# Kernel optimization log

Measured on AMD Instinct MI355X. Metric: run time of the kernel, lower is better.

## Reference

```python
import jax, jax.numpy as jnp
import numpy as np

H = 256  # hidden_size


def _lstm_cell(x, h, c, Wih, Whh, b):
    # PyTorch gate order: input, forget, cell(g), output
    gates = x @ Wih.T + h @ Whh.T + b  # (B, 4H)
    i, f, g, o = jnp.split(gates, 4, axis=-1)
    c_new = jax.nn.sigmoid(f) * c + jax.nn.sigmoid(i) * jnp.tanh(g)
    h_new = jax.nn.sigmoid(o) * jnp.tanh(c_new)
    return h_new, c_new


def setup_inputs() -> dict:
    key = jax.random.key(0)
    ks = jax.random.split(key, 9)
    B, D_in, T, H4 = 64, 64, 1024, 4 * H
    s = 0.05  # keep gates out of saturation
    return {
        "x": jax.random.normal(ks[0], (B, D_in, T), jnp.float32),
        # layer 0: input size 64; layers 1-2: input size 2*H (bidirectional concat)
        "Wih0": jax.random.normal(ks[1], (2, H4, D_in), jnp.float32) * s,
        "Whh0": jax.random.normal(ks[2], (2, H4, H), jnp.float32) * s,
        "b0": jax.random.normal(ks[3], (2, H4), jnp.float32) * s,  # b_ih + b_hh fused
        "Wih12": jax.random.normal(ks[4], (2, 2, H4, 2 * H), jnp.float32) * s,
        "Whh12": jax.random.normal(ks[5], (2, 2, H4, H), jnp.float32) * s,
        "b12": jax.random.normal(ks[6], (2, 2, H4), jnp.float32) * s,
        # Conv1d(1, 81, (256,1)) == per-timestep linear over the hidden dim
        "conv_w": jax.random.normal(ks[7], (81, H), jnp.float32) * s,
        "conv_b": jax.random.normal(ks[8], (81,), jnp.float32) * s,
    }


def reference(x, Wih0, Whh0, b0, Wih12, Whh12, b12, conv_w, conv_b):
    B = x.shape[0]
    seq = jnp.transpose(x, (2, 0, 1))  # (T, B, D_in) like x.permute(2,0,1)
    h0 = jnp.zeros((6, B, H), x.dtype)  # num_layers * num_directions = 6
    c0 = jnp.zeros((6, B, H), x.dtype)

    def step(carry, x_t):
        h, c = carry
        hs, cs = [], []
        inp = x_t  # single timestep fed to the (bi)LSTM: both dirs see the same input
        for l in range(3):
            outs = []
            for d in range(2):
                idx = 2 * l + d
                if l == 0:
                    Wih, Whh, b = Wih0[d], Whh0[d], b0[d]
                else:
                    Wih, Whh, b = Wih12[l - 1, d], Whh12[l - 1, d], b12[l - 1, d]
                hn, cn = _lstm_cell(inp, h[idx], c[idx], Wih, Whh, b)
                outs.append(hn)
                hs.append(hn)
                cs.append(cn)
            inp = jnp.concatenate(outs, axis=-1)  # (B, 2H) into next layer
        new_h = jnp.stack(hs)
        new_c = jnp.stack(cs)
        # h.view(L, 2, B, H)[-1, -1]: last layer, backward direction
        return (new_h, new_c), hs[-1]

    _, ys = jax.lax.scan(step, (h0, c0), seq)  # ys: (T, B, H)

    # y.permute(1,2,0).unsqueeze(1) -> conv (256,1) kernel -> squeeze(2):
    # logits[b, o, t] = sum_h conv_w[o, h] * ys[t, b, h] + conv_b[o]
    logits = jnp.einsum('tbh,oh->bot', ys, conv_w) + conv_b[None, :, None]
    probs = jax.nn.softmax(logits, axis=1)
    return jnp.argmax(probs, axis=1)  # (B, T) int
```

## Files before the change

### kernel.cpp

```cpp
#include <hip/hip_runtime.h>


#define H_ 256
#define B_ 64
#define T_ 1024
#define NBLK 256
#define NTHR 1024
#define HBUF 98304
#define NTICK 1026

#define OFF_GEN  0
#define OFF_ROOT 64
#define OFF_CNT  128
#define OFF_H    4096
#define OFF_XT   1048576
#define OFF_YS   17825792

__device__ __forceinline__ float sigf(float x) {
  return 1.0f / (1.0f + __expf(-x));
}
__device__ __forceinline__ float tanhf_(float x) {
  float e = __expf(-2.0f * fabsf(x));
  float r = (1.0f - e) / (1.0f + e);
  return x >= 0.0f ? r : -r;
}

__device__ __forceinline__ void llc_ld1(const float4* p, float4& r) {
  asm volatile(
      "global_load_dwordx4 %0, %1, off sc0 sc1\n\t"
      "s_waitcnt vmcnt(0)"
      : "=v"(r)
      : "v"(p)
      : "memory");
}
__device__ __forceinline__ void llc_ld4(const float4* p, float4& r0, float4& r1,
                                        float4& r2, float4& r3) {
  asm volatile(
      "global_load_dwordx4 %0, %4, off sc0 sc1\n\t"
      "global_load_dwordx4 %1, %4, off offset:1024 sc0 sc1\n\t"
      "global_load_dwordx4 %2, %4, off offset:2048 sc0 sc1\n\t"
      "global_load_dwordx4 %3, %4, off offset:3072 sc0 sc1\n\t"
      "s_waitcnt vmcnt(0)"
      : "=&v"(r0), "=&v"(r1), "=&v"(r2), "=&v"(r3)
      : "v"(p)
      : "memory");
}
__device__ __forceinline__ void llc_st1(float* p, float v) {
  asm volatile(
      "global_store_dword %0, %1, off sc0 sc1\n\t"
      "s_waitcnt vmcnt(0)" ::"v"(p),
      "v"(v)
      : "memory");
}
__device__ __forceinline__ void llc_st2(float* p1, float v1, float* p2, float v2) {
  asm volatile(
      "global_store_dword %0, %1, off sc0 sc1\n\t"
      "global_store_dword %2, %3, off sc0 sc1\n\t"
      "s_waitcnt vmcnt(0)" ::"v"(p1),
      "v"(v1), "v"(p2), "v"(v2)
      : "memory");
}

__global__ __launch_bounds__(64) void transpose_x(const float* __restrict__ x,
                                                  float* __restrict__ xT) {
  __shared__ float tile[64][65];
  const int k = blockIdx.y;
  const int t0 = blockIdx.x * 64;
  const int lane = threadIdx.x;
  for (int bi = 0; bi < 64; ++bi)
    tile[bi][lane] = x[bi * 65536 + k * 1024 + t0 + lane];
  __syncthreads();
  for (int ti = 0; ti < 64; ++ti)
    xT[(size_t)(t0 + ti) * 4096 + (k >> 2) * 256 + lane * 4 + (k & 3)] =
        tile[lane][ti];
}

__device__ __forceinline__ void body8(float* __restrict__ acc, const float4 av,
                                      const float* __restrict__ wb,
                                      const int ws, const int u0, const int k4) {
#pragma unroll
  for (int a = 0; a < 8; ++a) {
    const float* wp =
        wb + (size_t)((a & 3) * 256 + u0 + (a >> 2)) * ws + k4 * 4;
    float4 wq = *(const float4*)wp;
    acc[a] += wq.x * av.x + wq.y * av.y + wq.z * av.z + wq.w * av.w;
  }
}

__device__ __forceinline__ void seg8(float* __restrict__ acc, const int a,
                                     const int b, const float4* __restrict__ act,
                                     const int actOff,
                                     const float* __restrict__ wb, const int ws,
                                     const int u0, const int lane,
                                     const bool byp) {
  int k4 = a;
  for (; k4 + 4 <= b; k4 += 4) {
    const float4* p = act + (size_t)(k4 - actOff) * 64 + lane;
    float4 v0, v1, v2, v3;
    if (byp) {
      llc_ld4(p, v0, v1, v2, v3);
    } else {
      v0 = p[0];
      v1 = p[64];
      v2 = p[128];
      v3 = p[192];
    }
    body8(acc, v0, wb, ws, u0, k4 - actOff + 0);
    body8(acc, v1, wb, ws, u0, k4 - actOff + 1);
    body8(acc, v2, wb, ws, u0, k4 - actOff + 2);
    body8(acc, v3, wb, ws, u0, k4 - actOff + 3);
  }
  for (; k4 < b; ++k4) {
    const float4* p = act + (size_t)(k4 - actOff) * 64 + lane;
    float4 v;
    if (byp)
      llc_ld1(p, v);
    else
      v = *p;
    body8(acc, v, wb, ws, u0, k4 - actOff);
  }
}

__device__ __forceinline__ void task8(
    const int w, const int lane, const int tid, const int u0,
    const int K4, const int nA4,
    const float4* __restrict__ actA, const bool bypA,
    const float4* __restrict__ actB, const bool bypB,
    const float* __restrict__ wAb, const int wAs,
    const float* __restrict__ wBb, const int wBs,
    const float* __restrict__ bias,
    float* __restrict__ cst2,
    float* __restrict__ hcell,
    float* __restrict__ ysrow,
    float (*red)[64][12], const bool lastTask) {
  const int slice = K4 >> 4;
  const int lo = w * slice, hi = lo + slice;
  float acc[8] = {0.f, 0.f, 0.f, 0.f, 0.f, 0.f, 0.f, 0.f};

  {
    const int b4 = hi < nA4 ? hi : nA4;
    if (lo < b4) seg8(acc, lo, b4, actA, 0, wAb, wAs, u0, lane, bypA);
  }
  {
    const int a4 = lo > nA4 ? lo : nA4;
    if (a4 < hi) seg8(acc, a4, hi, actB, nA4, wBb, wBs, u0, lane, bypB);
  }

  *(float4*)&red[w][lane][0] = make_float4(acc[0], acc[1], acc[2], acc[3]);
  *(float4*)&red[w][lane][4] = make_float4(acc[4], acc[5], acc[6], acc[7]);
  __syncthreads();

  if (tid < 128) {
    const int uu = tid >> 6, b = tid & 63;
    float gi = bias[0 * 256 + u0 + uu];
    float gf = bias[1 * 256 + u0 + uu];
    float gg = bias[2 * 256 + u0 + uu];
    float go = bias[3 * 256 + u0 + uu];
#pragma unroll
    for (int ww = 0; ww < 16; ++ww) {
      float4 s = *(const float4*)&red[ww][b][uu * 4];
      gi += s.x; gf += s.y; gg += s.z; go += s.w;
    }
    float iv = sigf(gi), fv = sigf(gf), gv = tanhf_(gg), ov = sigf(go);
    float c = fv * cst2[uu * 64 + b] + iv * gv;
    cst2[uu * 64 + b] = c;
    float h = ov * tanhf_(c);
    const int u = u0 + uu;
    float* hp = hcell + (u >> 2) * 256 + b * 4 + (u & 3);
    if (ysrow)
      llc_st2(hp, h, ysrow + b * 256 + u, h);
    else
      llc_st1(hp, h);
  }
  if (!lastTask) __syncthreads();
}

__global__ __launch_bounds__(NTHR, 1) void lstm_persistent(
    const float* __restrict__ Wih0, const float* __restrict__ Whh0,
    const float* __restrict__ b0, const float* __restrict__ Wih12,
    const float* __restrict__ Whh12, const float* __restrict__ b12, char* wsb) {
  unsigned* gen = (unsigned*)(wsb + OFF_GEN);
  unsigned* root = (unsigned*)(wsb + OFF_ROOT);
  float* hb = (float*)(wsb + OFF_H);
  const float* xT = (const float*)(wsb + OFF_XT);
  float* ys = (float*)(wsb + OFF_YS);

  __shared__ float red[16][64][12];
  __shared__ float cst[3][2][64];

  const int bid = blockIdx.x;
  const int tid = threadIdx.x;
  const int lane = tid & 63;
  const int w = __builtin_amdgcn_readfirstlane(tid >> 6);
  const int d = bid >> 7;
  const int u0 = (bid & 127) * 2;

  if (tid < 384) ((float*)cst)[tid] = 0.f;
  __syncthreads();

  unsigned* mycnt = (unsigned*)(wsb + OFF_CNT + (size_t)(bid & 7) * 64);

  for (unsigned tick = 0; tick < NTICK; ++tick) {
    const float* R = hb + ((tick + 1) & 1) * HBUF;
    float* W = hb + (tick & 1) * HBUF;
    const float4* Rf4 = (const float4*)R;

    const bool has0 = tick < 1024;
    const bool has1 = tick >= 1 && tick < 1025;
    const bool has2 = tick >= 2;

    if (has0) {
      task8(w, lane, tid, u0, 80, 16,
            (const float4*)xT + (size_t)tick * 1024, false,
            Rf4 + (size_t)d * 4096, true,
            Wih0 + (size_t)d * 65536, 64,
            Whh0 + (size_t)d * 262144, 256,
            b0 + d * 1024, &cst[0][0][0], W + (size_t)d * 16384, nullptr, red,
            !(has1 || has2));
    }
    if (has1) {
      task8(w, lane, tid, u0, 192, 128,
            Rf4, true,
            Rf4 + (size_t)(2 + d) * 4096, true,
            Wih12 + (size_t)d * 524288, 512,
            Whh12 + (size_t)d * 262144, 256,
            b12 + d * 1024, &cst[1][0][0], W + (size_t)(2 + d) * 16384, nullptr,
            red, !has2);
    }
    if (has2) {
      const int t = (int)tick - 2;
      task8(w, lane, tid, u0, 192, 128,
            Rf4 + (size_t)2 * 4096, true,
            Rf4 + (size_t)(4 + d) * 4096, true,
            Wih12 + (size_t)(2 + d) * 524288, 512,
            Whh12 + (size_t)(2 + d) * 262144, 256,
            b12 + (2 + d) * 1024, &cst[2][0][0], W + (size_t)(4 + d) * 16384,
            (d == 1) ? (ys + (size_t)t * 16384) : nullptr, red, true);
    }

    __syncthreads();
    if (tid == 0) {
      unsigned old = __hip_atomic_fetch_add(mycnt, 1u, __ATOMIC_RELAXED,
                                            __HIP_MEMORY_SCOPE_AGENT);
      if (old == (tick + 1) * (NBLK / 8) - 1) {
        unsigned r = __hip_atomic_fetch_add(root, 1u, __ATOMIC_RELAXED,
                                            __HIP_MEMORY_SCOPE_AGENT);
        if (r == (tick + 1) * 8 - 1) {
          __hip_atomic_store(gen, tick + 1, __ATOMIC_RELAXED,
                             __HIP_MEMORY_SCOPE_AGENT);
        }
      }
      while (__hip_atomic_load(gen, __ATOMIC_RELAXED, __HIP_MEMORY_SCOPE_AGENT) <
             tick + 1) {
        __builtin_amdgcn_s_sleep(2);
      }
    }
    __syncthreads();
  }
}

__global__ __launch_bounds__(256) void conv_argmax(const float* __restrict__ yst,
                                                   const float* __restrict__ cw,
                                                   const float* __restrict__ cb,
                                                   int* __restrict__ out) {
  const int t = blockIdx.x;
  const int tid = threadIdx.x, lane = tid & 63, w = tid >> 6;
  const float* yrow = yst + (size_t)t * (B_ * H_) + lane * H_;
  float best = -3.4e38f;
  int bi = 0;
  for (int og = 0; og < 3; ++og) {
    float acc[8];
    int ov[8];
#pragma unroll
    for (int m = 0; m < 8; ++m) {
      int o = w + 32 * og + 4 * m;
      ov[m] = (o < 81) ? o : 80;
      acc[m] = (o < 81) ? cb[o] : -3.4e38f;
    }
    for (int uu = 0; uu < H_; uu += 4) {
      float4 y4 = *(const float4*)(yrow + uu);
#pragma unroll
      for (int m = 0; m < 8; ++m) {
        const float* wr = cw + ov[m] * H_ + uu;
        acc[m] += wr[0] * y4.x + wr[1] * y4.y + wr[2] * y4.z + wr[3] * y4.w;
      }
    }
#pragma unroll
    for (int m = 0; m < 8; ++m) {
      int o = w + 32 * og + 4 * m;
      if (o < 81 && acc[m] > best) {
        best = acc[m];
        bi = o;
      }
    }
  }
  __shared__ float sv[4][64];
  __shared__ int si[4][64];
  sv[w][lane] = best;
  si[w][lane] = bi;
  __syncthreads();
  if (tid < 64) {
    float bv = sv[0][tid];
    int bo = si[0][tid];
#pragma unroll
    for (int ww = 1; ww < 4; ++ww) {
      float v = sv[ww][tid];
      int o = si[ww][tid];
      if (v > bv || (v == bv && o < bo)) {
        bv = v;
        bo = o;
      }
    }
    out[tid * T_ + t] = bo;
  }
}

extern "C" void kernel_launch(void* const* d_in, const int* in_sizes, int n_in,
                              void* d_out, int out_size, void* d_ws,
                              size_t ws_size, hipStream_t stream) {
  const float* x = (const float*)d_in[0];
  const float* Wih0 = (const float*)d_in[1];
  const float* Whh0 = (const float*)d_in[2];
  const float* b0 = (const float*)d_in[3];
  const float* Wih12 = (const float*)d_in[4];
  const float* Whh12 = (const float*)d_in[5];
  const float* b12 = (const float*)d_in[6];
  const float* cw = (const float*)d_in[7];
  const float* cb = (const float*)d_in[8];
  int* out = (int*)d_out;
  char* wsb = (char*)d_ws;

  hipMemsetAsync(wsb, 0, OFF_H + 786432, stream);
  transpose_x<<<dim3(16, 64, 1), dim3(64, 1, 1), 0, stream>>>(
      x, (float*)(wsb + OFF_XT));
  lstm_persistent<<<dim3(NBLK, 1, 1), dim3(NTHR, 1, 1), 0, stream>>>(
      Wih0, Whh0, b0, Wih12, Whh12, b12, wsb);
  conv_argmax<<<dim3(T_, 1, 1), dim3(256, 1, 1), 0, stream>>>(
      (const float*)(wsb + OFF_YS), cw, cb, out);
}
```

Measured before the change: 18.41 ms.

## Stage per-block LSTM weights into LDS once with interleaved layout

Each persistent block now copies its slice of the input and recurrent weights for all three layers into shared memory once at kernel start, in a k4-major interleaved layout. The per-tick matvecs then read weights from LDS with contiguous float4 loads instead of strided global/L2 loads on every timestep. This removes repeated weight traffic across 1024 ticks but adds about 58KB of LDS per block and a one-time staging cost.

```diff
diff --git a/kernel.cpp b/kernel.cpp
--- a/kernel.cpp
+++ b/kernel.cpp
@@ -76,13 +76,12 @@
 }
 
 __device__ __forceinline__ void body8(float* __restrict__ acc, const float4 av,
-                                      const float* __restrict__ wb,
-                                      const int ws, const int u0, const int k4) {
+                                      const float* __restrict__ wl,
+                                      const int k4) {
+  const float* wp = wl + (size_t)k4 * 32;
 #pragma unroll
   for (int a = 0; a < 8; ++a) {
-    const float* wp =
-        wb + (size_t)((a & 3) * 256 + u0 + (a >> 2)) * ws + k4 * 4;
-    float4 wq = *(const float4*)wp;
+    float4 wq = *(const float4*)(wp + a * 4);
     acc[a] += wq.x * av.x + wq.y * av.y + wq.z * av.z + wq.w * av.w;
   }
 }
@@ -90,9 +89,8 @@
 __device__ __forceinline__ void seg8(float* __restrict__ acc, const int a,
                                      const int b, const float4* __restrict__ act,
                                      const int actOff,
-                                     const float* __restrict__ wb, const int ws,
-                                     const int u0, const int lane,
-                                     const bool byp) {
+                                     const float* __restrict__ wl,
+                                     const int lane, const bool byp) {
   int k4 = a;
   for (; k4 + 4 <= b; k4 += 4) {
     const float4* p = act + (size_t)(k4 - actOff) * 64 + lane;
@@ -105,10 +103,10 @@
       v2 = p[128];
       v3 = p[192];
     }
-    body8(acc, v0, wb, ws, u0, k4 - actOff + 0);
-    body8(acc, v1, wb, ws, u0, k4 - actOff + 1);
-    body8(acc, v2, wb, ws, u0, k4 - actOff + 2);
-    body8(acc, v3, wb, ws, u0, k4 - actOff + 3);
+    body8(acc, v0, wl, k4 + 0);
+    body8(acc, v1, wl, k4 + 1);
+    body8(acc, v2, wl, k4 + 2);
+    body8(acc, v3, wl, k4 + 3);
   }
   for (; k4 < b; ++k4) {
     const float4* p = act + (size_t)(k4 - actOff) * 64 + lane;
@@ -117,7 +115,7 @@
       llc_ld1(p, v);
     else
       v = *p;
-    body8(acc, v, wb, ws, u0, k4 - actOff);
+    body8(acc, v, wl, k4);
   }
 }
 
@@ -126,8 +124,7 @@
     const int K4, const int nA4,
     const float4* __restrict__ actA, const bool bypA,
     const float4* __restrict__ actB, const bool bypB,
-    const float* __restrict__ wAb, const int wAs,
-    const float* __restrict__ wBb, const int wBs,
+    const float* __restrict__ wl,
     const float* __restrict__ bias,
     float* __restrict__ cst2,
     float* __restrict__ hcell,
@@ -139,11 +136,11 @@
 
   {
     const int b4 = hi < nA4 ? hi : nA4;
-    if (lo < b4) seg8(acc, lo, b4, actA, 0, wAb, wAs, u0, lane, bypA);
+    if (lo < b4) seg8(acc, lo, b4, actA, 0, wl, lane, bypA);
   }
   {
     const int a4 = lo > nA4 ? lo : nA4;
-    if (a4 < hi) seg8(acc, a4, hi, actB, nA4, wBb, wBs, u0, lane, bypB);
+    if (a4 < hi) seg8(acc, a4, hi, actB, nA4, wl, lane, bypB);
   }
 
   *(float4*)&red[w][lane][0] = make_float4(acc[0], acc[1], acc[2], acc[3]);
@@ -187,6 +184,7 @@
 
   __shared__ float red[16][64][12];
   __shared__ float cst[3][2][64];
+  __shared__ float wlds[14848];
 
   const int bid = blockIdx.x;
   const int tid = threadIdx.x;
@@ -196,6 +194,26 @@
   const int u0 = (bid & 127) * 2;
 
   if (tid < 384) ((float*)cst)[tid] = 0.f;
+
+  auto stage = [&](const float* wA, int wAs, const float* wB, int wBs,
+                   int K4s, int NA4s, float* dst) {
+    const int nq = K4s * 8;
+    for (int idx = tid; idx < nq; idx += NTHR) {
+      const int a = idx / K4s;
+      const int k4 = idx - a * K4s;
+      const int row = (a & 3) * 256 + u0 + (a >> 2);
+      const float* src = (k4 < NA4s) ? (wA + (size_t)row * wAs + k4 * 4)
+                                     : (wB + (size_t)row * wBs + (k4 - NA4s) * 4);
+      float4 q = *(const float4*)src;
+      *(float4*)(dst + ((size_t)k4 * 8 + a) * 4) = q;
+    }
+  };
+  stage(Wih0 + (size_t)d * 65536, 64, Whh0 + (size_t)d * 262144, 256, 80, 16,
+        wlds);
+  stage(Wih12 + (size_t)d * 524288, 512, Whh12 + (size_t)d * 262144, 256, 192,
+        128, wlds + 2560);
+  stage(Wih12 + (size_t)(2 + d) * 524288, 512,
+        Whh12 + (size_t)(2 + d) * 262144, 256, 192, 128, wlds + 8704);
   __syncthreads();
 
   unsigned* mycnt = (unsigned*)(wsb + OFF_CNT + (size_t)(bid & 7) * 64);
@@ -213,28 +231,23 @@
       task8(w, lane, tid, u0, 80, 16,
             (const float4*)xT + (size_t)tick * 1024, false,
             Rf4 + (size_t)d * 4096, true,
-            Wih0 + (size_t)d * 65536, 64,
-            Whh0 + (size_t)d * 262144, 256,
-            b0 + d * 1024, &cst[0][0][0], W + (size_t)d * 16384, nullptr, red,
-            !(has1 || has2));
+            wlds, b0 + d * 1024, &cst[0][0][0],
+            W + (size_t)d * 16384, nullptr, red, !(has1 || has2));
     }
     if (has1) {
       task8(w, lane, tid, u0, 192, 128,
             Rf4, true,
             Rf4 + (size_t)(2 + d) * 4096, true,
-            Wih12 + (size_t)d * 524288, 512,
-            Whh12 + (size_t)d * 262144, 256,
-            b12 + d * 1024, &cst[1][0][0], W + (size_t)(2 + d) * 16384, nullptr,
-            red, !has2);
+            wlds + 2560, b12 + d * 1024, &cst[1][0][0],
+            W + (size_t)(2 + d) * 16384, nullptr, red, !has2);
     }
     if (has2) {
       const int t = (int)tick - 2;
       task8(w, lane, tid, u0, 192, 128,
             Rf4 + (size_t)2 * 4096, true,
             Rf4 + (size_t)(4 + d) * 4096, true,
-            Wih12 + (size_t)(2 + d) * 524288, 512,
-            Whh12 + (size_t)(2 + d) * 262144, 256,
-            b12 + (2 + d) * 1024, &cst[2][0][0], W + (size_t)(4 + d) * 16384,
+            wlds + 8704, b12 + (2 + d) * 1024, &cst[2][0][0],
+            W + (size_t)(4 + d) * 16384,
             (d == 1) ? (ys + (size_t)t * 16384) : nullptr, red, true);
     }
 
```

Result: no change. 18.39 ms (-0.1%).
